# Kernel optimization log

Hardware: AMD Instinct MI355X
Metric: run time of the kernel (lower is better)

## Reference

```python
import jax, jax.numpy as jnp
import numpy as np
import math

H = 512
NH = 8
HD = H // NH


def _lin_params(key, out_dim, in_dim):
    k1, k2 = jax.random.split(key)
    bound = 1.0 / math.sqrt(in_dim)
    w = jax.random.uniform(k1, (out_dim, in_dim), minval=-bound, maxval=bound, dtype=jnp.float32)
    b = jax.random.uniform(k2, (out_dim,), minval=-bound, maxval=bound, dtype=jnp.float32)
    return w, b


def setup_inputs() -> dict:
    key = jax.random.key(0)
    ks = jax.random.split(key, 16)
    B, L = 8, 1024
    inp = {
        'hidden_states': jax.random.normal(ks[0], (B, L, H), dtype=jnp.float32),
        'text': jax.random.normal(ks[1], (B, L, H), dtype=jnp.float32),
    }
    names = ['q_img', 'k_img', 'v_img', 'q_txt', 'k_txt', 'v_txt', 'out_img', 'out_txt']
    for i, n in enumerate(names):
        w, b = _lin_params(ks[2 + i], H, H)
        inp['w_' + n] = w
        inp['b_' + n] = b
    wcat, bcat = _lin_params(ks[10], H, 2 * H)
    inp['w_cat'] = wcat
    inp['b_cat'] = bcat
    # nn.MultiheadAttention params: in_proj [3H, H], out_proj [H, H]
    inp['in_proj_w'] = jax.random.normal(ks[11], (3 * H, H), dtype=jnp.float32) * (1.0 / math.sqrt(H))
    inp['in_proj_b'] = jnp.zeros((3 * H,), dtype=jnp.float32)
    pw, pb = _lin_params(ks[12], H, H)
    inp['out_proj_w'] = pw
    inp['out_proj_b'] = pb
    return inp


def _lin(x, w, b):
    return x @ w.T + b


def _heads(x):
    B, L, _ = x.shape
    return x.reshape(B, L, NH, HD).transpose(0, 2, 1, 3)  # [B, NH, L, HD]


def _attn(q, k, v):
    # q,k,v: [B, NH, L, HD]; dropout is identity in eval mode
    scores = jnp.einsum('bhqd,bhkd->bhqk', q, k) / math.sqrt(HD)
    probs = jax.nn.softmax(scores, axis=-1)
    ctx = jnp.einsum('bhqk,bhkd->bhqd', probs, v)
    B, _, L, _ = ctx.shape
    return ctx.transpose(0, 2, 1, 3).reshape(B, L, H)


def reference(hidden_states, text,
              w_q_img, b_q_img, w_k_img, b_k_img, w_v_img, b_v_img,
              w_q_txt, b_q_txt, w_k_txt, b_k_txt, w_v_txt, b_v_txt,
              w_out_img, b_out_img, w_out_txt, b_out_txt,
              w_cat, b_cat, in_proj_w, in_proj_b, out_proj_w, out_proj_b):
    q_img = _heads(_lin(hidden_states, w_q_img, b_q_img))
    k_img = _heads(_lin(hidden_states, w_k_img, b_k_img))
    v_img = _heads(_lin(hidden_states, w_v_img, b_v_img))
    q_txt = _heads(_lin(text, w_q_txt, b_q_txt))
    k_txt = _heads(_lin(text, w_k_txt, b_k_txt))
    v_txt = _heads(_lin(text, w_v_txt, b_v_txt))

    ctx_img = _attn(q_img, k_img, v_img)
    ctx_txt = _attn(q_txt, k_txt, v_txt)
    ctx_it = _attn(q_img, k_txt, v_txt)
    ctx_ti = _attn(q_txt, k_img, v_img)

    out_img = _lin((ctx_img + ctx_it) * 0.5, w_out_img, b_out_img)
    out_txt = _lin((ctx_txt + ctx_ti) * 0.5, w_out_txt, b_out_txt)
    out = _lin(jnp.concatenate([out_img, out_txt], axis=2), w_cat, b_cat)

    # attention pooling (nn.MultiheadAttention self-attention, batch-major math)
    qkv = _lin(out, in_proj_w, in_proj_b)
    q, k, v = jnp.split(qkv, 3, axis=-1)
    ctx = _attn(_heads(q), _heads(k), _heads(v))
    return _lin(ctx, out_proj_w, out_proj_b)
```

## Files before the change

kernel.cpp:

```cpp
#include <hip/hip_runtime.h>

typedef unsigned short u16;
typedef __attribute__((ext_vector_type(4))) unsigned short u16x4;
typedef __attribute__((ext_vector_type(8))) unsigned short u16x8;
typedef __attribute__((ext_vector_type(4))) float f32x4;
typedef __attribute__((ext_vector_type(8))) __bf16 bf16x8;
typedef __attribute__((ext_vector_type(4))) unsigned int u32x4;

#define WS_XH    0UL
#define WS_XT    8388608UL
#define WS_W     16777216UL
#define WS_BQI   24117248UL
#define WS_BQT   24123392UL
#define WS_QKVI  24129536UL
#define WS_QKVT  49295360UL
#define WS_VTI   74461184UL
#define WS_VTT   82849792UL
#define WS_CTXIA 91238400UL
#define WS_CTXTA 99627008UL
#define WS_OCAT  108015616UL
#define WS_OUT2  24129536UL
#define WS_QKVP  32518144UL
#define WS_VTP   57683968UL
#define WS_CTXP  66072576UL

#define SCALE_LOG2E_O8 0.18033688011112042f

__device__ __forceinline__ u16 f2bf(float f) {
  unsigned u = __float_as_uint(f);
  u += 0x7fffu + ((u >> 16) & 1u);
  return (u16)(u >> 16);
}
__device__ __forceinline__ float bf2f(u16 v) {
  return __uint_as_float(((unsigned)v) << 16);
}
__device__ __forceinline__ bf16x8 as_bf(u16x8 v) { return __builtin_bit_cast(bf16x8, v); }
__device__ __forceinline__ f32x4 mfma16(bf16x8 a, bf16x8 b, f32x4 c) {
  return __builtin_amdgcn_mfma_f32_16x16x32_bf16(a, b, c, 0, 0, 0);
}

__global__ __launch_bounds__(256) void cvt_f32_bf16(const float* __restrict__ s,
                                                    u16* __restrict__ d, int n) {
  int i = (blockIdx.x * 256 + threadIdx.x) * 4;
  if (i >= n) return;
  float4 v = *(const float4*)(s + i);
  u16x4 o;
  o[0] = f2bf(v.x); o[1] = f2bf(v.y); o[2] = f2bf(v.z); o[3] = f2bf(v.w);
  *(u16x4*)(d + i) = o;
}

__global__ __launch_bounds__(256) void prep_weights(
    const float* __restrict__ wqi, const float* __restrict__ wki, const float* __restrict__ wvi,
    const float* __restrict__ wqt, const float* __restrict__ wkt, const float* __restrict__ wvt,
    const float* __restrict__ woi, const float* __restrict__ wot,
    const float* __restrict__ wc,  const float* __restrict__ wip, const float* __restrict__ wop,
    const float* __restrict__ bqi, const float* __restrict__ bki, const float* __restrict__ bvi,
    const float* __restrict__ bqt, const float* __restrict__ bkt, const float* __restrict__ bvt,
    u16* __restrict__ wdst, float* __restrict__ bi, float* __restrict__ bt) {
  int i = blockIdx.x * 256 + threadIdx.x;
  if (i < 786432) {
    const float* s = i < 262144 ? wqi : (i < 524288 ? wki : wvi);
    wdst[i] = f2bf(s[i & 262143]);
  } else if (i < 1572864) {
    int j = i - 786432;
    const float* s = j < 262144 ? wqt : (j < 524288 ? wkt : wvt);
    wdst[i] = f2bf(s[j & 262143]);
  } else if (i < 1835008) wdst[i] = f2bf(woi[i - 1572864]);
  else if (i < 2097152)   wdst[i] = f2bf(wot[i - 1835008]);
  else if (i < 2621440)   wdst[i] = f2bf(wc [i - 2097152]);
  else if (i < 3407872)   wdst[i] = f2bf(wip[i - 2621440]);
  else if (i < 3670016)   wdst[i] = f2bf(wop[i - 3407872]);
  else if (i < 3671552) {
    int j = i - 3670016;
    bi[j] = j < 512 ? bqi[j] : (j < 1024 ? bki[j - 512] : bvi[j - 1024]);
  } else if (i < 3673088) {
    int j = i - 3671552;
    bt[j] = j < 512 ? bqt[j] : (j < 1024 ? bkt[j - 512] : bvt[j - 1024]);
  }
}

__global__ __launch_bounds__(256) void gemm_bf16(
    const u16* __restrict__ A, const u16* __restrict__ A2, int lda,
    const u16* __restrict__ W,
    const float* __restrict__ bias, u16* __restrict__ C, int ldc, int coff, int K,
    int f32out, int qcols, float qscale) {
  __shared__ __align__(16) u16 As[2][8 * 512];
  __shared__ __align__(16) u16 Bs[2][8 * 512];
  const int tid = threadIdx.x, lane = tid & 63, wv = tid >> 6;
  const int wm = wv >> 1, wn = wv & 1;
  const int ln15 = lane & 15;
  const int m0 = blockIdx.x * 128, n0 = blockIdx.y * 128;

  const int srow = lane & 15, skc = lane >> 4;
  const u16* gA0 = A + (long)(m0 + wv * 32 + srow) * lda + skc * 8;
  const u16* gA1 = gA0 + (long)16 * lda;
  const u16* gW0 = W + (long)(n0 + wv * 32 + srow) * K + skc * 8;
  const u16* gW1 = gW0 + (long)16 * K;
  const u16* gA20 = A2 + (long)(m0 + wv * 32 + srow) * lda + skc * 8;
  const u16* gA21 = gA20 + (long)16 * lda;

  f32x4 acc[4][4];
#pragma unroll
  for (int j = 0; j < 4; ++j) {
    float bv = bias[n0 + wn * 64 + j * 16 + ln15];
#pragma unroll
    for (int i = 0; i < 4; ++i) acc[i][j] = f32x4{bv, bv, bv, bv};
  }

  u16x8 ra0 = *(const u16x8*)(gA0);
  u16x8 ra1 = *(const u16x8*)(gA1);
  u16x8 rb0 = *(const u16x8*)(gW0);
  u16x8 rb1 = *(const u16x8*)(gW1);
  u16x8 rc0, rc1;
  if (A2) { rc0 = *(const u16x8*)(gA20); rc1 = *(const u16x8*)(gA21); }

  int buf = 0;
  for (int k0 = 0; k0 < K; k0 += 32, buf ^= 1) {
    u16x8 wa0 = ra0, wa1 = ra1;
    if (A2) {
#pragma unroll
      for (int u = 0; u < 8; ++u) {
        wa0[u] = f2bf(bf2f(ra0[u]) + bf2f(rc0[u]));
        wa1[u] = f2bf(bf2f(ra1[u]) + bf2f(rc1[u]));
      }
    }
    u16* la = As[buf] + (wv * 2) * 512;
    u16* lb = Bs[buf] + (wv * 2) * 512;
    *(u16x8*)(la + lane * 8) = wa0;
    *(u16x8*)(la + 512 + lane * 8) = wa1;
    *(u16x8*)(lb + lane * 8) = rb0;
    *(u16x8*)(lb + 512 + lane * 8) = rb1;
    if (k0 + 32 < K) {
      ra0 = *(const u16x8*)(gA0 + k0 + 32);
      ra1 = *(const u16x8*)(gA1 + k0 + 32);
      rb0 = *(const u16x8*)(gW0 + k0 + 32);
      rb1 = *(const u16x8*)(gW1 + k0 + 32);
      if (A2) { rc0 = *(const u16x8*)(gA20 + k0 + 32); rc1 = *(const u16x8*)(gA21 + k0 + 32); }
    }
    __syncthreads();

    bf16x8 af[4], bfr[4];
#pragma unroll
    for (int i = 0; i < 4; ++i)
      af[i] = as_bf(*(const u16x8*)(As[buf] + (wm * 4 + i) * 512 + lane * 8));
#pragma unroll
    for (int j = 0; j < 4; ++j)
      bfr[j] = as_bf(*(const u16x8*)(Bs[buf] + (wn * 4 + j) * 512 + lane * 8));
#pragma unroll
    for (int i = 0; i < 4; ++i)
#pragma unroll
      for (int j = 0; j < 4; ++j) acc[i][j] = mfma16(af[i], bfr[j], acc[i][j]);
  }
  const int quad = lane >> 4;
  const int qr4 = quad * 4;
  float colsc[4];
#pragma unroll
  for (int j = 0; j < 4; ++j)
    colsc[j] = (n0 + wn * 64 + j * 16 < qcols) ? qscale : 1.0f;
#pragma unroll
  for (int i = 0; i < 4; ++i)
#pragma unroll
    for (int r = 0; r < 4; ++r) {
      int row = m0 + wm * 64 + i * 16 + qr4 + r;
      long cidx = (long)row * ldc + coff + n0 + wn * 64 + ln15;
      if (f32out) {
        float* cf = (float*)C + cidx;
#pragma unroll
        for (int j = 0; j < 4; ++j) cf[j * 16] = acc[i][j][r] * colsc[j];
      } else {
        u16* cp = C + cidx;
#pragma unroll
        for (int j = 0; j < 4; ++j) cp[j * 16] = f2bf(acc[i][j][r] * colsc[j]);
      }
    }
}

__global__ __launch_bounds__(256) void transpose_v(const u16* __restrict__ src,
                                                   u16* __restrict__ dst) {
  __shared__ __align__(16) u16 T[64][72];
  const int t = threadIdx.x;
  const int l0 = blockIdx.x * 64, h = blockIdx.y, b = blockIdx.z;
  const u16* s = src + (long)b * 1024 * 1536 + 1024 + h * 64;
  {
    int l = t >> 2, co = (t & 3) * 16;
#pragma unroll
    for (int u = 0; u < 2; ++u)
      *(u16x8*)(&T[l][co + u * 8]) = *(const u16x8*)(s + (long)(l0 + l) * 1536 + co + u * 8);
  }
  __syncthreads();
  {
    int d = t >> 2, lo = (t & 3) * 16;
    u16 tmp[16];
#pragma unroll
    for (int u = 0; u < 16; ++u) tmp[u] = T[lo + u][d];
    u16x8 v0, v1;
#pragma unroll
    for (int u = 0; u < 8; ++u) { v0[u] = tmp[u]; v1[u] = tmp[8 + u]; }
    u16* dp = dst + (long)((b * 8 + h) * 64 + d) * 1024 + l0 + lo;
    *(u16x8*)dp = v0;
    *(u16x8*)(dp + 8) = v1;
  }
}

template <int NQF>
__global__ __launch_bounds__(256) void attn_flash(
    const u16* __restrict__ Q, int ldq,
    const u16* __restrict__ KA, const u16* __restrict__ VTA,
    const u16* __restrict__ KB, const u16* __restrict__ VTB, int ldk,
    u16* __restrict__ OA, u16* __restrict__ OB, int ldo, float outscale) {
  __shared__ __align__(16) u16 Kt[32][72];
  __shared__ __align__(16) u16 Vt[64][40];
  __shared__ __align__(16) u16 Pw[4][NQF * 16][56];
  const int tid = threadIdx.x, lane = tid & 63, wv = tid >> 6;
  const int ln15 = lane & 15, quad = lane >> 4, q8 = quad * 8;
  const int h = blockIdx.y, b = blockIdx.z;

  const u16 *K, *VT;
  u16* O;
  int qtile;
  if (KB != nullptr) {
    qtile = blockIdx.x >> 1;
    int phase = blockIdx.x & 1;
    K = phase ? KB : KA;
    VT = phase ? VTB : VTA;
    O = phase ? OB : OA;
  } else {
    qtile = blockIdx.x;
    K = KA; VT = VTA; O = OA;
  }
  const long qrow = (long)b * 1024 + qtile * (NQF * 64) + wv * (NQF * 16);

  bf16x8 qf[NQF][2];
#pragma unroll
  for (int qi = 0; qi < NQF; ++qi) {
    const u16* qp = Q + (qrow + qi * 16 + ln15) * ldq + h * 64;
    qf[qi][0] = as_bf(*(const u16x8*)(qp + q8));
    qf[qi][1] = as_bf(*(const u16x8*)(qp + 32 + q8));
  }

  u16x8 ones_u;
#pragma unroll
  for (int j = 0; j < 8; ++j) ones_u[j] = 0x3F80;
  const bf16x8 onesb = as_bf(ones_u);

  const int kk = tid >> 3, dc = (tid & 7) * 8;
  const int rp = ((kk & 1) << 4) | (kk >> 1);
  const int vd = tid >> 2, ko = (tid & 3) * 8;
  const u16* Kbase = K + ((long)b * 1024 + kk) * ldk + h * 64 + dc;
  const u16* Vbase = VT + ((long)((b * 8 + h) * 64 + vd)) * 1024 + ko;

  f32x4 o[NQF][4];
  f32x4 lacc[NQF];
#pragma unroll
  for (int qi = 0; qi < NQF; ++qi) {
    lacc[qi] = f32x4{0.f, 0.f, 0.f, 0.f};
#pragma unroll
    for (int j = 0; j < 4; ++j) o[qi][j] = f32x4{0.f, 0.f, 0.f, 0.f};
  }

  u32x4 kreg = *(const u32x4*)(Kbase);
  u32x4 vreg = *(const u32x4*)(Vbase);

  for (int k0 = 0; k0 < 1024; k0 += 32) {
    *(u32x4*)(&Kt[rp][dc]) = kreg;
    *(u32x4*)(&Vt[vd][ko]) = vreg;
    __syncthreads();
    if (k0 + 32 < 1024) {
      kreg = *(const u32x4*)(Kbase + (long)(k0 + 32) * ldk);
      vreg = *(const u32x4*)(Vbase + (k0 + 32));
    }

    f32x4 s[2][NQF];
#pragma unroll
    for (int kb = 0; kb < 2; ++kb) {
      bf16x8 b0 = as_bf(*(const u16x8*)(&Kt[kb * 16 + ln15][q8]));
      bf16x8 b1 = as_bf(*(const u16x8*)(&Kt[kb * 16 + ln15][32 + q8]));
#pragma unroll
      for (int qi = 0; qi < NQF; ++qi) {
        f32x4 z = f32x4{0.f, 0.f, 0.f, 0.f};
        z = mfma16(qf[qi][0], b0, z);
        z = mfma16(qf[qi][1], b1, z);
        s[kb][qi] = z;
      }
    }

#pragma unroll
    for (int qi = 0; qi < NQF; ++qi)
#pragma unroll
      for (int r = 0; r < 4; ++r) {
        float p0 = __builtin_amdgcn_exp2f(s[0][qi][r]);
        float p1 = __builtin_amdgcn_exp2f(s[1][qi][r]);
        unsigned u0 = __float_as_uint(p0) + 0x8000u;
        unsigned u1 = __float_as_uint(p1) + 0x8000u;
        unsigned pk = __builtin_amdgcn_perm(u1, u0, 0x07060302);
        *(unsigned*)(&Pw[wv][qi * 16 + quad * 4 + r][2 * ln15]) = pk;
      }
    bf16x8 pa[NQF];
#pragma unroll
    for (int qi = 0; qi < NQF; ++qi) {
      pa[qi] = as_bf(*(const u16x8*)(&Pw[wv][qi * 16 + ln15][q8]));
      lacc[qi] = mfma16(pa[qi], onesb, lacc[qi]);
    }
#pragma unroll
    for (int j = 0; j < 4; ++j) {
      bf16x8 vb = as_bf(*(const u16x8*)(&Vt[j * 16 + ln15][q8]));
#pragma unroll
      for (int qi = 0; qi < NQF; ++qi) o[qi][j] = mfma16(pa[qi], vb, o[qi][j]);
    }
    __syncthreads();
  }

#pragma unroll
  for (int qi = 0; qi < NQF; ++qi)
#pragma unroll
    for (int r = 0; r < 4; ++r) {
      float inv = outscale / lacc[qi][r];
      long row = qrow + qi * 16 + quad * 4 + r;
#pragma unroll
      for (int j = 0; j < 4; ++j)
        O[row * ldo + h * 64 + j * 16 + ln15] = f2bf(o[qi][j][r] * inv);
    }
}

extern "C" void kernel_launch(void* const* d_in, const int* in_sizes, int n_in,
                              void* d_out, int out_size, void* d_ws, size_t ws_size,
                              hipStream_t stream) {
  const float* hidden = (const float*)d_in[0];
  const float* text   = (const float*)d_in[1];
  const float* wqi = (const float*)d_in[2];  const float* bqi = (const float*)d_in[3];
  const float* wki = (const float*)d_in[4];  const float* bki = (const float*)d_in[5];
  const float* wvi = (const float*)d_in[6];  const float* bvi = (const float*)d_in[7];
  const float* wqt = (const float*)d_in[8];  const float* bqt = (const float*)d_in[9];
  const float* wkt = (const float*)d_in[10]; const float* bkt = (const float*)d_in[11];
  const float* wvt = (const float*)d_in[12]; const float* bvt = (const float*)d_in[13];
  const float* woi = (const float*)d_in[14]; const float* boi = (const float*)d_in[15];
  const float* wot = (const float*)d_in[16]; const float* bot = (const float*)d_in[17];
  const float* wc  = (const float*)d_in[18]; const float* bc  = (const float*)d_in[19];
  const float* wip = (const float*)d_in[20]; const float* bip = (const float*)d_in[21];
  const float* wop = (const float*)d_in[22]; const float* bop = (const float*)d_in[23];

  char* ws = (char*)d_ws;
  u16* XH    = (u16*)(ws + WS_XH);
  u16* XT    = (u16*)(ws + WS_XT);
  u16* WB    = (u16*)(ws + WS_W);
  float* BQI = (float*)(ws + WS_BQI);
  float* BQT = (float*)(ws + WS_BQT);
  u16* QKVI  = (u16*)(ws + WS_QKVI);
  u16* QKVT  = (u16*)(ws + WS_QKVT);
  u16* VTI   = (u16*)(ws + WS_VTI);
  u16* VTT   = (u16*)(ws + WS_VTT);
  u16* CTXIA = (u16*)(ws + WS_CTXIA);
  u16* CTXIB = (u16*)(ws + WS_XH);
  u16* CTXTA = (u16*)(ws + WS_CTXTA);
  u16* CTXTB = (u16*)(ws + WS_XT);
  u16* OCAT  = (u16*)(ws + WS_OCAT);
  u16* OUT2  = (u16*)(ws + WS_OUT2);
  u16* QKVP  = (u16*)(ws + WS_QKVP);
  u16* VTP   = (u16*)(ws + WS_VTP);
  u16* CTXP  = (u16*)(ws + WS_CTXP);

  u16* WQKVI = WB;
  u16* WQKVT = WB + 786432;
  u16* WOUTI = WB + 1572864;
  u16* WOUTT = WB + 1835008;
  u16* WCAT  = WB + 2097152;
  u16* WINP  = WB + 2621440;
  u16* WOUTP = WB + 3407872;

  const int NACT = 8192 * 512;

  cvt_f32_bf16<<<dim3(NACT / 1024), 256, 0, stream>>>(hidden, XH, NACT);
  cvt_f32_bf16<<<dim3(NACT / 1024), 256, 0, stream>>>(text, XT, NACT);
  prep_weights<<<dim3(14348), 256, 0, stream>>>(wqi, wki, wvi, wqt, wkt, wvt, woi, wot,
                                                wc, wip, wop, bqi, bki, bvi, bqt, bkt, bvt,
                                                WB, BQI, BQT);
  gemm_bf16<<<dim3(64, 12), 256, 0, stream>>>(XH, nullptr, 512, WQKVI, BQI, QKVI, 1536, 0, 512,
                                              0, 512, SCALE_LOG2E_O8);
  gemm_bf16<<<dim3(64, 12), 256, 0, stream>>>(XT, nullptr, 512, WQKVT, BQT, QKVT, 1536, 0, 512,
                                              0, 512, SCALE_LOG2E_O8);
  transpose_v<<<dim3(16, 8, 8), 256, 0, stream>>>(QKVI, VTI);
  transpose_v<<<dim3(16, 8, 8), 256, 0, stream>>>(QKVT, VTT);
  attn_flash<2><<<dim3(16, 8, 8), 256, 0, stream>>>(QKVI, 1536, QKVI + 512, VTI,
                                                    QKVT + 512, VTT, 1536,
                                                    CTXIA, CTXIB, 512, 0.5f);
  attn_flash<2><<<dim3(16, 8, 8), 256, 0, stream>>>(QKVT, 1536, QKVT + 512, VTT,
                                                    QKVI + 512, VTI, 1536,
                                                    CTXTA, CTXTB, 512, 0.5f);
  gemm_bf16<<<dim3(64, 4), 256, 0, stream>>>(CTXIA, CTXIB, 512, WOUTI, boi, OCAT, 1024, 0, 512,
                                             0, 0, 1.0f);
  gemm_bf16<<<dim3(64, 4), 256, 0, stream>>>(CTXTA, CTXTB, 512, WOUTT, bot, OCAT, 1024, 512, 512,
                                             0, 0, 1.0f);
  gemm_bf16<<<dim3(64, 4), 256, 0, stream>>>(OCAT, nullptr, 1024, WCAT, bc, OUT2, 512, 0, 1024,
                                             0, 0, 1.0f);
  gemm_bf16<<<dim3(64, 12), 256, 0, stream>>>(OUT2, nullptr, 512, WINP, bip, QKVP, 1536, 0, 512,
                                              0, 512, SCALE_LOG2E_O8);
  transpose_v<<<dim3(16, 8, 8), 256, 0, stream>>>(QKVP, VTP);
  attn_flash<1><<<dim3(16, 8, 8), 256, 0, stream>>>(QKVP, 1536, QKVP + 512, VTP,
                                                    nullptr, nullptr, 1536,
                                                    CTXP, nullptr, 512, 1.0f);
  gemm_bf16<<<dim3(64, 4), 256, 0, stream>>>(CTXP, nullptr, 512, WOUTP, bop, (u16*)d_out, 512,
                                             0, 512, 1, 0, 1.0f);
}
```

Measured before the change: 436.6 us.

## Fuse V transpose into QKV GEMM epilogue and keep softmax probs in registers

The QKV projection GEMM now writes the V columns directly in transposed [B,NH,HD,L] layout, which removes the three separate transpose_v launches and their extra round-trip through memory. The flash attention kernel swaps MFMA operand roles so the score tiles come out transposed. That lets exp2 results be packed into bf16 B-operands in registers, dropping the per-wave LDS staging buffer for P. The K staging permutation is removed and the V staging writes are rearranged to match the new operand layout. The risks are layout correctness of the swapped operands and uncoalesced 8-byte column stores in the GEMM epilogue.

```diff
diff --git a/kernel.cpp b/kernel.cpp
--- a/kernel.cpp
+++ b/kernel.cpp
@@ -5,6 +5,7 @@
 typedef __attribute__((ext_vector_type(8))) unsigned short u16x8;
 typedef __attribute__((ext_vector_type(4))) float f32x4;
 typedef __attribute__((ext_vector_type(8))) __bf16 bf16x8;
+typedef __attribute__((ext_vector_type(2))) unsigned int u32x2;
 typedef __attribute__((ext_vector_type(4))) unsigned int u32x4;
 
 #define WS_XH    0UL
@@ -37,6 +38,11 @@
 __device__ __forceinline__ bf16x8 as_bf(u16x8 v) { return __builtin_bit_cast(bf16x8, v); }
 __device__ __forceinline__ f32x4 mfma16(bf16x8 a, bf16x8 b, f32x4 c) {
   return __builtin_amdgcn_mfma_f32_16x16x32_bf16(a, b, c, 0, 0, 0);
+}
+__device__ __forceinline__ unsigned pack_bf2(float lo, float hi) {
+  unsigned a = __float_as_uint(lo) + 0x8000u;
+  unsigned b = __float_as_uint(hi) + 0x8000u;
+  return __builtin_amdgcn_perm(b, a, 0x07060302);
 }
 
 __global__ __launch_bounds__(256) void cvt_f32_bf16(const float* __restrict__ s,
@@ -83,7 +89,7 @@
     const u16* __restrict__ A, const u16* __restrict__ A2, int lda,
     const u16* __restrict__ W,
     const float* __restrict__ bias, u16* __restrict__ C, int ldc, int coff, int K,
-    int f32out, int qcols, float qscale) {
+    int f32out, int qcols, float qscale, u16* __restrict__ vtout) {
   __shared__ __align__(16) u16 As[2][8 * 512];
   __shared__ __align__(16) u16 Bs[2][8 * 512];
   const int tid = threadIdx.x, lane = tid & 63, wv = tid >> 6;
@@ -153,6 +159,25 @@
   }
   const int quad = lane >> 4;
   const int qr4 = quad * 4;
+  if (vtout && n0 >= 1024) {
+#pragma unroll
+    for (int j = 0; j < 4; ++j) {
+      int col = n0 + wn * 64 + j * 16 + ln15;
+      int dg = col - 1024;
+      long vtrow = ((long)0 * 8 + (dg >> 6)) * 64 + (dg & 63);
+#pragma unroll
+      for (int i = 0; i < 4; ++i) {
+        int row0 = m0 + wm * 64 + i * 16 + qr4;
+        long vr = ((long)(row0 >> 10) * 8 + (dg >> 6)) * 64 + (dg & 63);
+        u16x4 ov;
+#pragma unroll
+        for (int r = 0; r < 4; ++r) ov[r] = f2bf(acc[i][j][r]);
+        *(u16x4*)(vtout + vr * 1024 + (row0 & 1023)) = ov;
+      }
+      (void)vtrow;
+    }
+    return;
+  }
   float colsc[4];
 #pragma unroll
   for (int j = 0; j < 4; ++j)
@@ -173,33 +198,6 @@
         for (int j = 0; j < 4; ++j) cp[j * 16] = f2bf(acc[i][j][r] * colsc[j]);
       }
     }
-}
-
-__global__ __launch_bounds__(256) void transpose_v(const u16* __restrict__ src,
-                                                   u16* __restrict__ dst) {
-  __shared__ __align__(16) u16 T[64][72];
-  const int t = threadIdx.x;
-  const int l0 = blockIdx.x * 64, h = blockIdx.y, b = blockIdx.z;
-  const u16* s = src + (long)b * 1024 * 1536 + 1024 + h * 64;
-  {
-    int l = t >> 2, co = (t & 3) * 16;
-#pragma unroll
-    for (int u = 0; u < 2; ++u)
-      *(u16x8*)(&T[l][co + u * 8]) = *(const u16x8*)(s + (long)(l0 + l) * 1536 + co + u * 8);
-  }
-  __syncthreads();
-  {
-    int d = t >> 2, lo = (t & 3) * 16;
-    u16 tmp[16];
-#pragma unroll
-    for (int u = 0; u < 16; ++u) tmp[u] = T[lo + u][d];
-    u16x8 v0, v1;
-#pragma unroll
-    for (int u = 0; u < 8; ++u) { v0[u] = tmp[u]; v1[u] = tmp[8 + u]; }
-    u16* dp = dst + (long)((b * 8 + h) * 64 + d) * 1024 + l0 + lo;
-    *(u16x8*)dp = v0;
-    *(u16x8*)(dp + 8) = v1;
-  }
 }
 
 template <int NQF>
@@ -210,7 +208,6 @@
     u16* __restrict__ OA, u16* __restrict__ OB, int ldo, float outscale) {
   __shared__ __align__(16) u16 Kt[32][72];
   __shared__ __align__(16) u16 Vt[64][40];
-  __shared__ __align__(16) u16 Pw[4][NQF * 16][56];
   const int tid = threadIdx.x, lane = tid & 63, wv = tid >> 6;
   const int ln15 = lane & 15, quad = lane >> 4, q8 = quad * 8;
   const int h = blockIdx.y, b = blockIdx.z;
@@ -244,8 +241,9 @@
   const bf16x8 onesb = as_bf(ones_u);
 
   const int kk = tid >> 3, dc = (tid & 7) * 8;
-  const int rp = ((kk & 1) << 4) | (kk >> 1);
-  const int vd = tid >> 2, ko = (tid & 3) * 8;
+  const int vd = tid >> 2;
+  const int ko = (tid & 3) * 8;
+  const int vs0 = ((tid & 1) << 4) | ((tid & 2) << 1);
   const u16* Kbase = K + ((long)b * 1024 + kk) * ldk + h * 64 + dc;
   const u16* Vbase = VT + ((long)((b * 8 + h) * 64 + vd)) * 1024 + ko;
 
@@ -262,64 +260,70 @@
   u32x4 vreg = *(const u32x4*)(Vbase);
 
   for (int k0 = 0; k0 < 1024; k0 += 32) {
-    *(u32x4*)(&Kt[rp][dc]) = kreg;
-    *(u32x4*)(&Vt[vd][ko]) = vreg;
+    *(u32x4*)(&Kt[kk][dc]) = kreg;
+    u32x2 vlo = {vreg[0], vreg[1]}, vhi = {vreg[2], vreg[3]};
+    *(u32x2*)(&Vt[vd][vs0]) = vlo;
+    *(u32x2*)(&Vt[vd][vs0 + 8]) = vhi;
     __syncthreads();
     if (k0 + 32 < 1024) {
       kreg = *(const u32x4*)(Kbase + (long)(k0 + 32) * ldk);
       vreg = *(const u32x4*)(Vbase + (k0 + 32));
     }
 
-    f32x4 s[2][NQF];
-#pragma unroll
-    for (int kb = 0; kb < 2; ++kb) {
-      bf16x8 b0 = as_bf(*(const u16x8*)(&Kt[kb * 16 + ln15][q8]));
-      bf16x8 b1 = as_bf(*(const u16x8*)(&Kt[kb * 16 + ln15][32 + q8]));
+    f32x4 st[2][NQF];
+#pragma unroll
+    for (int kt = 0; kt < 2; ++kt) {
+      bf16x8 ka0 = as_bf(*(const u16x8*)(&Kt[kt * 16 + ln15][q8]));
+      bf16x8 ka1 = as_bf(*(const u16x8*)(&Kt[kt * 16 + ln15][32 + q8]));
 #pragma unroll
       for (int qi = 0; qi < NQF; ++qi) {
         f32x4 z = f32x4{0.f, 0.f, 0.f, 0.f};
-        z = mfma16(qf[qi][0], b0, z);
-        z = mfma16(qf[qi][1], b1, z);
-        s[kb][qi] = z;
+        z = mfma16(ka0, qf[qi][0], z);
+        z = mfma16(ka1, qf[qi][1], z);
+        st[kt][qi] = z;
       }
     }
 
-#pragma unroll
-    for (int qi = 0; qi < NQF; ++qi)
-#pragma unroll
-      for (int r = 0; r < 4; ++r) {
-        float p0 = __builtin_amdgcn_exp2f(s[0][qi][r]);
-        float p1 = __builtin_amdgcn_exp2f(s[1][qi][r]);
-        unsigned u0 = __float_as_uint(p0) + 0x8000u;
-        unsigned u1 = __float_as_uint(p1) + 0x8000u;
-        unsigned pk = __builtin_amdgcn_perm(u1, u0, 0x07060302);
-        *(unsigned*)(&Pw[wv][qi * 16 + quad * 4 + r][2 * ln15]) = pk;
-      }
-    bf16x8 pa[NQF];
+    bf16x8 pb[NQF];
 #pragma unroll
     for (int qi = 0; qi < NQF; ++qi) {
-      pa[qi] = as_bf(*(const u16x8*)(&Pw[wv][qi * 16 + ln15][q8]));
-      lacc[qi] = mfma16(pa[qi], onesb, lacc[qi]);
+      float p00 = __builtin_amdgcn_exp2f(st[0][qi][0]);
+      float p01 = __builtin_amdgcn_exp2f(st[0][qi][1]);
+      float p02 = __builtin_amdgcn_exp2f(st[0][qi][2]);
+      float p03 = __builtin_amdgcn_exp2f(st[0][qi][3]);
+      float p10 = __builtin_amdgcn_exp2f(st[1][qi][0]);
+      float p11 = __builtin_amdgcn_exp2f(st[1][qi][1]);
+      float p12 = __builtin_amdgcn_exp2f(st[1][qi][2]);
+      float p13 = __builtin_amdgcn_exp2f(st[1][qi][3]);
+      u32x4 pk;
+      pk[0] = pack_bf2(p00, p01);
+      pk[1] = pack_bf2(p02, p03);
+      pk[2] = pack_bf2(p10, p11);
+      pk[3] = pack_bf2(p12, p13);
+      pb[qi] = as_bf(__builtin_bit_cast(u16x8, pk));
+      lacc[qi] = mfma16(onesb, pb[qi], lacc[qi]);
     }
 #pragma unroll
     for (int j = 0; j < 4; ++j) {
-      bf16x8 vb = as_bf(*(const u16x8*)(&Vt[j * 16 + ln15][q8]));
-#pragma unroll
-      for (int qi = 0; qi < NQF; ++qi) o[qi][j] = mfma16(pa[qi], vb, o[qi][j]);
+      bf16x8 av = as_bf(*(const u16x8*)(&Vt[j * 16 + ln15][q8]));
+#pragma unroll
+      for (int qi = 0; qi < NQF; ++qi) o[qi][j] = mfma16(av, pb[qi], o[qi][j]);
     }
     __syncthreads();
   }
 
 #pragma unroll
-  for (int qi = 0; qi < NQF; ++qi)
-#pragma unroll
-    for (int r = 0; r < 4; ++r) {
-      float inv = outscale / lacc[qi][r];
-      long row = qrow + qi * 16 + quad * 4 + r;
-#pragma unroll
-      for (int j = 0; j < 4; ++j)
-        O[row * ldo + h * 64 + j * 16 + ln15] = f2bf(o[qi][j][r] * inv);
-    }
+  for (int qi = 0; qi < NQF; ++qi) {
+    float inv = outscale / lacc[qi][0];
+    long row = qrow + qi * 16 + ln15;
+#pragma unroll
+    for (int j = 0; j < 4; ++j) {
+      u16x4 ov;
+#pragma unroll
+      for (int r = 0; r < 4; ++r) ov[r] = f2bf(o[qi][j][r] * inv);
+      *(u16x4*)(O + row * ldo + h * 64 + j * 16 + quad * 4) = ov;
+    }
+  }
 }
 
 extern "C" void kernel_launch(void* const* d_in, const int* in_sizes, int n_in,
@@ -375,11 +379,9 @@
                                                 wc, wip, wop, bqi, bki, bvi, bqt, bkt, bvt,
                                                 WB, BQI, BQT);
   gemm_bf16<<<dim3(64, 12), 256, 0, stream>>>(XH, nullptr, 512, WQKVI, BQI, QKVI, 1536, 0, 512,
-                                              0, 512, SCALE_LOG2E_O8);
+                                              0, 512, SCALE_LOG2E_O8, VTI);
   gemm_bf16<<<dim3(64, 12), 256, 0, stream>>>(XT, nullptr, 512, WQKVT, BQT, QKVT, 1536, 0, 512,
-                                              0, 512, SCALE_LOG2E_O8);
-  transpose_v<<<dim3(16, 8, 8), 256, 0, stream>>>(QKVI, VTI);
-  transpose_v<<<dim3(16, 8, 8), 256, 0, stream>>>(QKVT, VTT);
+                                              0, 512, SCALE_LOG2E_O8, VTT);
   attn_flash<2><<<dim3(16, 8, 8), 256, 0, stream>>>(QKVI, 1536, QKVI + 512, VTI,
                                                     QKVT + 512, VTT, 1536,
                                                     CTXIA, CTXIB, 512, 0.5f);
@@ -387,17 +389,16 @@
                                                     QKVI + 512, VTI, 1536,
                                                     CTXTA, CTXTB, 512, 0.5f);
   gemm_bf16<<<dim3(64, 4), 256, 0, stream>>>(CTXIA, CTXIB, 512, WOUTI, boi, OCAT, 1024, 0, 512,
-                                             0, 0, 1.0f);
+                                             0, 0, 1.0f, nullptr);
   gemm_bf16<<<dim3(64, 4), 256, 0, stream>>>(CTXTA, CTXTB, 512, WOUTT, bot, OCAT, 1024, 512, 512,
-                                             0, 0, 1.0f);
+                                             0, 0, 1.0f, nullptr);
   gemm_bf16<<<dim3(64, 4), 256, 0, stream>>>(OCAT, nullptr, 1024, WCAT, bc, OUT2, 512, 0, 1024,
-                                             0, 0, 1.0f);
+                                             0, 0, 1.0f, nullptr);
   gemm_bf16<<<dim3(64, 12), 256, 0, stream>>>(OUT2, nullptr, 512, WINP, bip, QKVP, 1536, 0, 512,
-                                              0, 512, SCALE_LOG2E_O8);
-  transpose_v<<<dim3(16, 8, 8), 256, 0, stream>>>(QKVP, VTP);
+                                              0, 512, SCALE_LOG2E_O8, VTP);
   attn_flash<1><<<dim3(16, 8, 8), 256, 0, stream>>>(QKVP, 1536, QKVP + 512, VTP,
                                                     nullptr, nullptr, 1536,
                                                     CTXP, nullptr, 512, 1.0f);
   gemm_bf16<<<dim3(64, 4), 256, 0, stream>>>(CTXP, nullptr, 512, WOUTP, bop, (u16*)d_out, 512,
-                                             0, 512, 1, 0, 1.0f);
-}
+                                             0, 512, 1, 0, 1.0f, nullptr);
+}
```

New measurement: 402.8 us. -7.7%, faster.
